# Kernel tuning notes

Hardware: AMD Instinct MI355X
Metric: run time of the kernel (lower is better)

## Reference

```python
import jax, jax.numpy as jnp
import numpy as np

BN_EPS = 1e-5


def setup_inputs() -> dict:
    key = jax.random.key(0)
    ks = jax.random.split(key, 10)
    B, C2, Hh, Ww = 4, 64, 64, 64  # in_channels=128, C/2=64
    C = 2 * C2
    inp = {
        "H": jax.random.normal(ks[0], (B, C2, Hh, Ww), jnp.float32),
        "L": jax.random.normal(ks[1], (B, C2, Hh, Ww), jnp.float32),
        # 1x1 convs stored as [out, in] matrices
        "theta_w": jax.random.normal(ks[2], (C2, C), jnp.float32) * (1.0 / np.sqrt(C)),
        "theta_b": jnp.zeros((C2,), jnp.float32),
        "phi_w": jax.random.normal(ks[3], (C2, C), jnp.float32) * (1.0 / np.sqrt(C)),
        "phi_b": jnp.zeros((C2,), jnp.float32),
        "g_w": jax.random.normal(ks[4], (C2, C2), jnp.float32) * (1.0 / np.sqrt(C2)),
        "g_b": jnp.zeros((C2,), jnp.float32),
        # 3x3 conv of CBR block, OIHW
        "conv_w": jax.random.normal(ks[5], (C2, C2, 3, 3), jnp.float32) * (1.0 / np.sqrt(C2 * 9)),
        "conv_b": jnp.zeros((C2,), jnp.float32),
        # BatchNorm (inference-mode) params
        "bn_gamma": jnp.ones((C2,), jnp.float32),
        "bn_beta": jnp.zeros((C2,), jnp.float32),
        "bn_mean": jnp.zeros((C2,), jnp.float32),
        "bn_var": jnp.ones((C2,), jnp.float32),
    }
    return inp


def reference(H, L, theta_w, theta_b, phi_w, phi_b, g_w, g_b,
              conv_w, conv_b, bn_gamma, bn_beta, bn_mean, bn_var):
    B, C2, h, w = L.shape
    N = h * w
    HL = jnp.concatenate([H, L], axis=1)  # [B, C, h, w]
    # 1x1 conv projections as channel matmuls
    A = jnp.einsum('oc,bchw->bohw', theta_w, HL) + theta_b[:, None, None]  # [B,C2,h,w]
    Bm = jnp.einsum('oc,bchw->bohw', phi_w, HL) + phi_b[:, None, None]
    A = A.reshape(B, C2, N).transpose(0, 2, 1)   # [B, N, C2]
    Bm = Bm.reshape(B, C2, N)                    # [B, C2, N]
    M = jnp.einsum('bnc,bcm->bnm', A, Bm)        # [B, N, N], unscaled
    M = jax.nn.softmax(M, axis=1)                # softmax over FIRST spatial axis (dim=1)
    D = jnp.einsum('oc,bchw->bohw', g_w, L) + g_b[:, None, None]
    D = D.reshape(B, C2, N)                      # [B, C2, N]
    E = jnp.einsum('bcn,bnm->bcm', D, M)         # [B, C2, N]
    E = E.reshape(B, C2, h, w)
    # CBR: conv3x3(pad=1) -> BatchNorm (inference) -> ReLU
    F = jax.lax.conv_general_dilated(
        E, conv_w, window_strides=(1, 1), padding='SAME',
        dimension_numbers=('NCHW', 'OIHW', 'NCHW')) + conv_b[None, :, None, None]
    F = (F - bn_mean[None, :, None, None]) * jax.lax.rsqrt(bn_var + BN_EPS)[None, :, None, None]
    F = F * bn_gamma[None, :, None, None] + bn_beta[None, :, None, None]
    F = jax.nn.relu(F)
    return H + F
```

## Files before the change

### kernel.cpp

```cpp
#include <hip/hip_runtime.h>

typedef __bf16 bf16;
typedef unsigned short u16;
typedef __attribute__((ext_vector_type(8))) __bf16 bf16x8;
typedef __attribute__((ext_vector_type(16))) float f32x16;
typedef __attribute__((ext_vector_type(2))) unsigned int uint2v;
typedef __attribute__((ext_vector_type(4))) unsigned int uint4v;

#define MFMA32(a, b, c) __builtin_amdgcn_mfma_f32_32x32x16_bf16(a, b, c, 0, 0, 0)

__device__ __forceinline__ u16 bbits(float f) {
  bf16 h = (bf16)f;
  return __builtin_bit_cast(u16, h);
}
__device__ __forceinline__ float bf2f(u16 u) {
  return (float)__builtin_bit_cast(bf16, u);
}
__device__ __forceinline__ bf16x8 ldg16(const u16* p) {
  return *reinterpret_cast<const bf16x8*>(p);
}
__device__ __forceinline__ bf16x8 ld_p8(const u16* p) {
  uint2v a = *reinterpret_cast<const uint2v*>(p);
  uint2v b = *reinterpret_cast<const uint2v*>(p + 4);
  uint4v u;
  u.x = a.x; u.y = a.y; u.z = b.x; u.w = b.y;
  return __builtin_bit_cast(bf16x8, u);
}
__device__ __forceinline__ void split8(const float* xv, bf16x8& hi, bf16x8& lo) {
  uint4v hv, lv;
#pragma unroll
  for (int jp = 0; jp < 4; ++jp) {
    float a0 = xv[2 * jp], a1 = xv[2 * jp + 1];
    u16 h0 = bbits(a0), h1 = bbits(a1);
    u16 l0 = bbits(a0 - bf2f(h0)), l1 = bbits(a1 - bf2f(h1));
    unsigned hh = (unsigned)h0 | ((unsigned)h1 << 16);
    unsigned ll = (unsigned)l0 | ((unsigned)l1 << 16);
    if (jp == 0) { hv.x = hh; lv.x = ll; }
    else if (jp == 1) { hv.y = hh; lv.y = ll; }
    else if (jp == 2) { hv.z = hh; lv.z = ll; }
    else { hv.w = hh; lv.w = ll; }
  }
  hi = __builtin_bit_cast(bf16x8, hv);
  lo = __builtin_bit_cast(bf16x8, lv);
}


__global__ __launch_bounds__(256) void pa_prep(
    const float* __restrict__ cw, const float* __restrict__ cbias,
    const float* __restrict__ gamma, const float* __restrict__ beta,
    const float* __restrict__ mean, const float* __restrict__ var,
    const float* __restrict__ tw, const float* __restrict__ pw, const float* __restrict__ gw,
    u16* __restrict__ Wt, float* __restrict__ bnA, float* __restrict__ bnB,
    u16* __restrict__ Wth, u16* __restrict__ Wtl,
    u16* __restrict__ Wph, u16* __restrict__ Wpl,
    u16* __restrict__ Wgh, u16* __restrict__ Wgl) {
  int i = blockIdx.x * 256 + threadIdx.x;
  if (i < 36864) {
    int ci = i & 63, co = (i >> 6) & 63, s = i >> 12;
    Wt[(s * 64 + co) * 64 + ci] = bbits(cw[(co * 64 + ci) * 9 + s]);
  }
  if (i < 16384) {
    int ii = i & 8191;
    int j = ii & 7, l = (ii >> 3) & 63, f = ii >> 9;
    int out = (f & 1) * 32 + (l & 31);
    int in = (f >> 1) * 16 + (l >> 5) * 8 + j;
    const float* W = (i < 8192) ? tw : pw;
    float v = W[out * 128 + in];
    u16 h = bbits(v);
    u16 lo = bbits(v - bf2f(h));
    if (i < 8192) { Wth[ii] = h; Wtl[ii] = lo; }
    else { Wph[ii] = h; Wpl[ii] = lo; }
  } else if (i < 20480) {
    int ii = i - 16384;
    int j = ii & 7, l = (ii >> 3) & 63, f = ii >> 9;
    int out = (f & 1) * 32 + (l & 31);
    int in = (f >> 1) * 16 + (l >> 5) * 8 + j;
    float v = gw[out * 64 + in];
    u16 h = bbits(v);
    Wgh[ii] = h;
    Wgl[ii] = bbits(v - bf2f(h));
  }
  if (i < 64) {
    float rs = rsqrtf(var[i] + 1e-5f);
    float A = gamma[i] * rs;
    bnA[i] = A;
    bnB[i] = (cbias[i] - mean[i]) * A + beta[i];
  }
}

template <bool LO>
__device__ __forceinline__ void store_qk_swz(const f32x16& a0, const f32x16& a1,
                                             const float* __restrict__ bias,
                                             u16* __restrict__ Hi, u16* __restrict__ Lo,
                                             int base, int l31, int q2) {
#pragma unroll
  for (int mt = 0; mt < 2; ++mt) {
    const f32x16& A = mt ? a1 : a0;
#pragma unroll
    for (int rq = 0; rq < 4; ++rq) {
      int ch = mt * 32 + rq * 8 + q2 * 4;
      float4 bb = *reinterpret_cast<const float4*>(bias + ch);
      float v0 = A[rq * 4 + 0] + bb.x;
      float v1 = A[rq * 4 + 1] + bb.y;
      float v2 = A[rq * 4 + 2] + bb.z;
      float v3 = A[rq * 4 + 3] + bb.w;
      int off = base + ((mt * 2 + (rq >> 1)) * 64 + l31 + 32 * (rq & 1)) * 8 + q2 * 4;
      u16 h0 = bbits(v0), h1 = bbits(v1), h2 = bbits(v2), h3 = bbits(v3);
      uint2v hv;
      hv.x = (unsigned)h0 | ((unsigned)h1 << 16);
      hv.y = (unsigned)h2 | ((unsigned)h3 << 16);
      *reinterpret_cast<uint2v*>(Hi + off) = hv;
      if (LO) {
        u16 l0 = bbits(v0 - bf2f(h0)), l1 = bbits(v1 - bf2f(h1));
        u16 l2 = bbits(v2 - bf2f(h2)), l3 = bbits(v3 - bf2f(h3));
        uint2v lv;
        lv.x = (unsigned)l0 | ((unsigned)l1 << 16);
        lv.y = (unsigned)l2 | ((unsigned)l3 << 16);
        *reinterpret_cast<uint2v*>(Lo + off) = lv;
      }
    }
  }
}

template <int NS>
__device__ __forceinline__ void gemm3(const u16* __restrict__ Wh, const u16* __restrict__ Wl,
                                      const bf16x8* Bh, const bf16x8* Bl,
                                      int lane, f32x16& a0, f32x16& a1) {
#pragma unroll
  for (int s = 0; s < NS; ++s) {
    bf16x8 w0h = ldg16(Wh + ((s * 2 + 0) * 64 + lane) * 8);
    bf16x8 w0l = ldg16(Wl + ((s * 2 + 0) * 64 + lane) * 8);
    bf16x8 w1h = ldg16(Wh + ((s * 2 + 1) * 64 + lane) * 8);
    bf16x8 w1l = ldg16(Wl + ((s * 2 + 1) * 64 + lane) * 8);
    a0 = MFMA32(w0h, Bh[s], a0);
    a0 = MFMA32(w0h, Bl[s], a0);
    a0 = MFMA32(w0l, Bh[s], a0);
    a1 = MFMA32(w1h, Bh[s], a1);
    a1 = MFMA32(w1h, Bl[s], a1);
    a1 = MFMA32(w1l, Bh[s], a1);
  }
}

__global__ __launch_bounds__(384, 2) void pa_proj(
    const float* __restrict__ H, const float* __restrict__ L,
    const float* __restrict__ tb, const float* __restrict__ pb, const float* __restrict__ gb,
    const u16* __restrict__ Wth, const u16* __restrict__ Wtl,
    const u16* __restrict__ Wph, const u16* __restrict__ Wpl,
    const u16* __restrict__ Wgh, const u16* __restrict__ Wgl,
    u16* __restrict__ Qh, u16* __restrict__ Ql,
    u16* __restrict__ Kh, u16* __restrict__ V) {
  int b = blockIdx.x >> 6;
  int tile64 = blockIdx.x & 63;
  int w = threadIdx.x >> 6;
  int lane = threadIdx.x & 63;
  int l31 = lane & 31, q2 = lane >> 5;
  int half = w & 1, role = w >> 1;
  int tile32 = tile64 * 2 + half;
  int n = tile32 * 32 + l31;
  int base = tile32 * 2048;

  if (role < 2) {
    bf16x8 Bh[8], Bl[8];
#pragma unroll
    for (int s = 0; s < 8; ++s) {
      const float* src = (s < 4) ? (H + (b * 64 + s * 16) * 4096)
                                 : (L + (b * 64 + (s - 4) * 16) * 4096);
      const float* pp = src + (q2 * 8) * 4096 + n;
      float xv[8];
#pragma unroll
      for (int j = 0; j < 8; ++j) xv[j] = pp[j * 4096];
      split8(xv, Bh[s], Bl[s]);
    }
    f32x16 a0 = {}, a1 = {};
    if (role == 0) {
      gemm3<8>(Wth, Wtl, Bh, Bl, lane, a0, a1);
      store_qk_swz<false>(a0, a1, tb, Kh + b * 262144, (u16*)nullptr, base, l31, q2);
    } else {
      gemm3<8>(Wph, Wpl, Bh, Bl, lane, a0, a1);
      store_qk_swz<true>(a0, a1, pb, Qh + b * 262144, Ql + b * 262144, base, l31, q2);
    }
  } else {
    bf16x8 Bh[4], Bl[4];
#pragma unroll
    for (int s = 0; s < 4; ++s) {
      const float* pp = L + (b * 64 + s * 16 + q2 * 8) * 4096 + n;
      float xv[8];
#pragma unroll
      for (int j = 0; j < 8; ++j) xv[j] = pp[j * 4096];
      split8(xv, Bh[s], Bl[s]);
    }
    f32x16 a0 = {}, a1 = {};
    gemm3<4>(Wgh, Wgl, Bh, Bl, lane, a0, a1);
    u16* Vb = V + b * 262144;
    int kch = (l31 >> 4) & 1, q2v = (l31 >> 3) & 1, jn = l31 & 7;
#pragma unroll
    for (int mt = 0; mt < 2; ++mt) {
      const f32x16& A = mt ? a1 : a0;
#pragma unroll
      for (int rq = 0; rq < 4; ++rq) {
        int ch = mt * 32 + rq * 8 + q2 * 4;
        float4 bb = *reinterpret_cast<const float4*>(gb + ch);
        float vv[4] = {A[rq * 4 + 0] + bb.x, A[rq * 4 + 1] + bb.y,
                       A[rq * 4 + 2] + bb.z, A[rq * 4 + 3] + bb.w};
#pragma unroll
        for (int i2 = 0; i2 < 4; ++i2) {
          int c31 = rq * 8 + q2 * 4 + i2;
          int lane_v = c31 + 32 * q2v;
          Vb[(((tile32 * 2 + kch) * 2 + mt) * 64 + lane_v) * 8 + jn] = bbits(vv[i2]);
        }
      }
    }
  }
}

__global__ __launch_bounds__(512, 4) void pa_flash(
    const u16* __restrict__ Qhg, const u16* __restrict__ Qlg,
    const u16* __restrict__ Khg, const u16* __restrict__ Vg, u16* __restrict__ E) {
  __shared__ __align__(16) char smem[18432];
  u16* Pb = (u16*)smem;
  float* Obuf = (float*)smem;
  float* MLm = (float*)(smem + 8448);
  float* MLl = (float*)(smem + 9472);
  float* Lst = (float*)(smem + 10496);

  int tid = threadIdx.x;
  int w = tid >> 6, lane = tid & 63;
  int l31 = lane & 31, q2 = lane >> 5;
  int b = blockIdx.x >> 7, mt = blockIdx.x & 127;
  int m0 = mt * 32;
  int bq = b * 4096;
  const u16* Qb = Qhg + b * 262144;
  const u16* Qlb = Qlg + b * 262144;
  const u16* Kb = Khg + b * 262144;
  const u16* Vb = Vg + b * 262144;

  bf16x8 qh[4], ql[4];
#pragma unroll
  for (int kc = 0; kc < 4; ++kc) {
    qh[kc] = ldg16(Qb + ((mt * 4 + kc) * 64 + lane) * 8);
    ql[kc] = ldg16(Qlb + ((mt * 4 + kc) * 64 + lane) * 8);
  }

  f32x16 accO[2] = {};
  float Mm = 0.f, Ll = 0.f;
  u16* mypb = Pb + w * (32 * 36);
  u16* prow = mypb + l31 * 36;

#pragma unroll 1
  for (int it = 0; it < 16; ++it) {
    int tile = it * 8 + w;

    bf16x8 kh[4];
#pragma unroll
    for (int kc = 0; kc < 4; ++kc) kh[kc] = ldg16(Kb + ((tile * 4 + kc) * 64 + lane) * 8);
    bf16x8 vf[2][2];
#pragma unroll
    for (int kch = 0; kch < 2; ++kch)
#pragma unroll
      for (int cbi = 0; cbi < 2; ++cbi)
        vf[cbi][kch] = ldg16(Vb + (((tile * 2 + kch) * 2 + cbi) * 64 + lane) * 8);

    f32x16 a = {};
#pragma unroll
    for (int kc = 0; kc < 4; ++kc) {
      a = MFMA32(kh[kc], qh[kc], a);
      a = MFMA32(kh[kc], ql[kc], a);
    }
    if (it == 0) {
      float tmax = a[0];
#pragma unroll
      for (int r = 1; r < 16; ++r) tmax = fmaxf(tmax, a[r]);
      tmax = fmaxf(tmax, __shfl_xor(tmax, 32, 64));
      Mm = tmax;
    }
    float pv[16];
    float psum = 0.f;
#pragma unroll
    for (int r = 0; r < 16; ++r) {
      pv[r] = __expf(a[r] - Mm);
      psum += pv[r];
    }
    psum += __shfl_xor(psum, 32, 64);
    Ll += psum;
#pragma unroll
    for (int rq = 0; rq < 4; ++rq) {
      unsigned lo = (unsigned)bbits(pv[rq * 4 + 0]) | ((unsigned)bbits(pv[rq * 4 + 1]) << 16);
      unsigned hi = (unsigned)bbits(pv[rq * 4 + 2]) | ((unsigned)bbits(pv[rq * 4 + 3]) << 16);
      uint2v uu;
      uu.x = lo;
      uu.y = hi;
      *reinterpret_cast<uint2v*>(prow + rq * 8 + q2 * 4) = uu;
    }
    bf16x8 p0 = ld_p8(prow + q2 * 8);
    bf16x8 p1 = ld_p8(prow + 16 + q2 * 8);
    accO[0] = MFMA32(vf[0][0], p0, accO[0]);
    accO[0] = MFMA32(vf[0][1], p1, accO[0]);
    accO[1] = MFMA32(vf[1][0], p0, accO[1]);
    accO[1] = MFMA32(vf[1][1], p1, accO[1]);
  }

  __syncthreads();
  if (q2 == 0) {
    MLm[w * 32 + l31] = Mm;
    MLl[w * 32 + l31] = Ll;
  }
  __syncthreads();
  float M = MLm[l31];
  for (int ww = 1; ww < 8; ++ww) M = fmaxf(M, MLm[ww * 32 + l31]);
  float ls = 0.f;
  for (int ww = 0; ww < 8; ++ww) ls += MLl[ww * 32 + l31] * __expf(MLm[ww * 32 + l31] - M);
  float mysc = __expf(Mm - M);
  if (w == 0 && q2 == 0) Lst[l31] = ls;
  for (int ww = 0; ww < 8; ++ww) {
    if (w == ww) {
#pragma unroll
      for (int cbi = 0; cbi < 2; ++cbi)
#pragma unroll
        for (int r = 0; r < 16; ++r) {
          int c = cbi * 32 + (r & 3) + 8 * (r >> 2) + 4 * q2;
          float* dst = &Obuf[c * 33 + l31];
          float v = accO[cbi][r] * mysc;
          if (ww == 0)
            *dst = v;
          else
            *dst += v;
        }
    }
    __syncthreads();
  }
  int em = tid >> 4, ec0 = (tid & 15) * 4;
  float invl = 1.0f / Lst[em];
  float v0 = Obuf[(ec0 + 0) * 33 + em] * invl;
  float v1 = Obuf[(ec0 + 1) * 33 + em] * invl;
  float v2 = Obuf[(ec0 + 2) * 33 + em] * invl;
  float v3 = Obuf[(ec0 + 3) * 33 + em] * invl;
  uint2v u0;
  u0.x = (unsigned)bbits(v0) | ((unsigned)bbits(v1) << 16);
  u0.y = (unsigned)bbits(v2) | ((unsigned)bbits(v3) << 16);
  *reinterpret_cast<uint2v*>(E + (bq + m0 + em) * 64 + ec0) = u0;
}

__global__ __launch_bounds__(256) void pa_conv(
    const u16* __restrict__ E, const u16* __restrict__ Wt,
    const float* __restrict__ bnA, const float* __restrict__ bnB,
    const float* __restrict__ H, float* __restrict__ out) {
  __shared__ u16 Er[3][66 * 68];
  int tid = threadIdx.x;
  int blk = blockIdx.x;
  int b = blk >> 6, y = blk & 63;
  int lane = tid & 63;
  int l31 = lane & 31, q2 = lane >> 5;
  int wv = tid >> 6;
  int cbi = wv >> 1, mb = wv & 1;
  int s0 = (y == 0) ? 1 : 0;
  int s1 = (y == 63) ? 1 : 2;

  for (int s = s0; s <= s1; ++s) {
    int yy = y + s - 1;
#pragma unroll
    for (int rep = 0; rep < 2; ++rep) {
      int id = rep * 256 + tid;
      int x = id >> 3, co = (id & 7) * 8;
      const uint2v* src = reinterpret_cast<const uint2v*>(E + ((b * 4096 + yy * 64 + x) * 64 + co));
      uint2v a = src[0], b4 = src[1];
      u16* d = &Er[s][(x + 1) * 68 + co];
      *reinterpret_cast<uint2v*>(d) = a;
      *reinterpret_cast<uint2v*>(d + 4) = b4;
    }
  }
  if (tid < 96) {
    int s = tid >> 5, side = (tid >> 4) & 1, co = (tid & 15) * 4;
    uint2v z;
    z.x = 0;
    z.y = 0;
    *reinterpret_cast<uint2v*>(&Er[s][(side ? 65 : 0) * 68 + co]) = z;
  }
  __syncthreads();

  f32x16 acc = {};
  for (int s = s0; s <= s1; ++s) {
#pragma unroll
    for (int dx = 0; dx < 3; ++dx)
#pragma unroll
      for (int kc = 0; kc < 4; ++kc) {
        bf16x8 a = ldg16(Wt + ((s * 3 + dx) * 64 + cbi * 32 + l31) * 64 + kc * 16 + q2 * 8);
        const u16* pbr = &Er[s][(mb * 32 + l31 + dx) * 68 + kc * 16 + q2 * 8];
        bf16x8 bb = ld_p8(pbr);
        acc = MFMA32(a, bb, acc);
      }
  }
#pragma unroll
  for (int r = 0; r < 16; ++r) {
    int c = cbi * 32 + (r & 3) + 8 * (r >> 2) + 4 * q2;
    int x = mb * 32 + l31;
    float v = acc[r] * bnA[c] + bnB[c];
    v = fmaxf(v, 0.f);
    int idx = ((b * 64 + c) * 64 + y) * 64 + x;
    out[idx] = H[idx] + v;
  }
}

extern "C" void kernel_launch(void* const* d_in, const int* in_sizes, int n_in,
                              void* d_out, int out_size, void* d_ws, size_t ws_size,
                              hipStream_t stream) {
  (void)in_sizes; (void)n_in; (void)out_size; (void)ws_size;
  const float* H = (const float*)d_in[0];
  const float* L = (const float*)d_in[1];
  const float* tw = (const float*)d_in[2];
  const float* tb = (const float*)d_in[3];
  const float* pw = (const float*)d_in[4];
  const float* pb = (const float*)d_in[5];
  const float* gw = (const float*)d_in[6];
  const float* gb = (const float*)d_in[7];
  const float* cw = (const float*)d_in[8];
  const float* cb = (const float*)d_in[9];
  const float* gamma = (const float*)d_in[10];
  const float* beta = (const float*)d_in[11];
  const float* mean = (const float*)d_in[12];
  const float* var = (const float*)d_in[13];

  const int NC = 16384 * 64;
  u16* Qh = (u16*)d_ws;
  u16* Ql = Qh + NC;
  u16* Kh = Ql + NC;
  u16* Vv = Kh + NC;
  u16* Eb = Vv + NC;
  u16* Wt = Eb + NC;
  float* bnA = (float*)(Wt + 36864);
  float* bnB = bnA + 64;
  u16* Wth = (u16*)(bnB + 64);
  u16* Wtl = Wth + 8192;
  u16* Wph = Wtl + 8192;
  u16* Wpl = Wph + 8192;
  u16* Wgh = Wpl + 8192;
  u16* Wgl = Wgh + 4096;

  pa_prep<<<144, 256, 0, stream>>>(cw, cb, gamma, beta, mean, var, tw, pw, gw,
                                   Wt, bnA, bnB, Wth, Wtl, Wph, Wpl, Wgh, Wgl);
  pa_proj<<<256, 384, 0, stream>>>(H, L, tb, pb, gb, Wth, Wtl, Wph, Wpl, Wgh, Wgl,
                                   Qh, Ql, Kh, Vv);
  pa_flash<<<512, 512, 0, stream>>>(Qh, Ql, Kh, Vv, Eb);
  pa_conv<<<256, 256, 0, stream>>>(Eb, Wt, bnA, bnB, H, (float*)d_out);
}
```

Baseline: 133.4 us.

## Trim split-bf16 terms, register P exchange, K prefetch, split-K conv

Drops the low-weight bf16 term for the theta and g projections, so those GEMMs issue two MFMAs per step instead of three. The flash kernel now moves P between lanes with cross-lane shuffles instead of an LDS round-trip, and prefetches the next K tile into registers. The conv kernel uses 512 threads with a split-K over channel chunks reduced through shared memory, and reads weights in an MFMA-fragment layout. Dropping the low weight terms slightly reduces projection precision. The conv split-K adds a barrier and extra LDS traffic.

```diff
diff --git a/kernel.cpp b/kernel.cpp
--- a/kernel.cpp
+++ b/kernel.cpp
@@ -25,6 +25,9 @@
   uint4v u;
   u.x = a.x; u.y = a.y; u.z = b.x; u.w = b.y;
   return __builtin_bit_cast(bf16x8, u);
+}
+__device__ __forceinline__ unsigned packbf(float a, float b) {
+  return (unsigned)bbits(a) | ((unsigned)bbits(b) << 16);
 }
 __device__ __forceinline__ void split8(const float* xv, bf16x8& hi, bf16x8& lo) {
   uint4v hv, lv;
@@ -57,7 +60,10 @@
   int i = blockIdx.x * 256 + threadIdx.x;
   if (i < 36864) {
     int ci = i & 63, co = (i >> 6) & 63, s = i >> 12;
-    Wt[(s * 64 + co) * 64 + ci] = bbits(cw[(co * 64 + ci) * 9 + s]);
+    int kc = ci >> 4, q2c = (ci >> 3) & 1, j = ci & 7;
+    int lane = q2c * 32 + (co & 31);
+    int cbi = co >> 5;
+    Wt[(((s * 4 + kc) * 2 + cbi) * 64 + lane) * 8 + j] = bbits(cw[(co * 64 + ci) * 9 + s]);
   }
   if (i < 16384) {
     int ii = i & 8191;
@@ -141,12 +147,26 @@
   }
 }
 
+template <int NS>
+__device__ __forceinline__ void gemm2(const u16* __restrict__ Wh,
+                                      const bf16x8* Bh, const bf16x8* Bl,
+                                      int lane, f32x16& a0, f32x16& a1) {
+#pragma unroll
+  for (int s = 0; s < NS; ++s) {
+    bf16x8 w0h = ldg16(Wh + ((s * 2 + 0) * 64 + lane) * 8);
+    bf16x8 w1h = ldg16(Wh + ((s * 2 + 1) * 64 + lane) * 8);
+    a0 = MFMA32(w0h, Bh[s], a0);
+    a0 = MFMA32(w0h, Bl[s], a0);
+    a1 = MFMA32(w1h, Bh[s], a1);
+    a1 = MFMA32(w1h, Bl[s], a1);
+  }
+}
+
 __global__ __launch_bounds__(384, 2) void pa_proj(
     const float* __restrict__ H, const float* __restrict__ L,
     const float* __restrict__ tb, const float* __restrict__ pb, const float* __restrict__ gb,
-    const u16* __restrict__ Wth, const u16* __restrict__ Wtl,
-    const u16* __restrict__ Wph, const u16* __restrict__ Wpl,
-    const u16* __restrict__ Wgh, const u16* __restrict__ Wgl,
+    const u16* __restrict__ Wth, const u16* __restrict__ Wph, const u16* __restrict__ Wpl,
+    const u16* __restrict__ Wgh,
     u16* __restrict__ Qh, u16* __restrict__ Ql,
     u16* __restrict__ Kh, u16* __restrict__ V) {
   int b = blockIdx.x >> 6;
@@ -173,7 +193,7 @@
     }
     f32x16 a0 = {}, a1 = {};
     if (role == 0) {
-      gemm3<8>(Wth, Wtl, Bh, Bl, lane, a0, a1);
+      gemm2<8>(Wth, Bh, Bl, lane, a0, a1);
       store_qk_swz<false>(a0, a1, tb, Kh + b * 262144, (u16*)nullptr, base, l31, q2);
     } else {
       gemm3<8>(Wph, Wpl, Bh, Bl, lane, a0, a1);
@@ -190,7 +210,7 @@
       split8(xv, Bh[s], Bl[s]);
     }
     f32x16 a0 = {}, a1 = {};
-    gemm3<4>(Wgh, Wgl, Bh, Bl, lane, a0, a1);
+    gemm2<4>(Wgh, Bh, Bl, lane, a0, a1);
     u16* Vb = V + b * 262144;
     int kch = (l31 >> 4) & 1, q2v = (l31 >> 3) & 1, jn = l31 & 7;
 #pragma unroll
@@ -216,12 +236,10 @@
 __global__ __launch_bounds__(512, 4) void pa_flash(
     const u16* __restrict__ Qhg, const u16* __restrict__ Qlg,
     const u16* __restrict__ Khg, const u16* __restrict__ Vg, u16* __restrict__ E) {
-  __shared__ __align__(16) char smem[18432];
-  u16* Pb = (u16*)smem;
-  float* Obuf = (float*)smem;
-  float* MLm = (float*)(smem + 8448);
-  float* MLl = (float*)(smem + 9472);
-  float* Lst = (float*)(smem + 10496);
+  __shared__ float Obuf[64 * 33];
+  __shared__ float MLm[8 * 32];
+  __shared__ float MLl[8 * 32];
+  __shared__ float Lst[32];
 
   int tid = threadIdx.x;
   int w = tid >> 6, lane = tid & 63;
@@ -243,16 +261,15 @@
 
   f32x16 accO[2] = {};
   float Mm = 0.f, Ll = 0.f;
-  u16* mypb = Pb + w * (32 * 36);
-  u16* prow = mypb + l31 * 36;
+
+  bf16x8 kh[4];
+#pragma unroll
+  for (int kc = 0; kc < 4; ++kc) kh[kc] = ldg16(Kb + ((w * 4 + kc) * 64 + lane) * 8);
 
 #pragma unroll 1
   for (int it = 0; it < 16; ++it) {
     int tile = it * 8 + w;
 
-    bf16x8 kh[4];
-#pragma unroll
-    for (int kc = 0; kc < 4; ++kc) kh[kc] = ldg16(Kb + ((tile * 4 + kc) * 64 + lane) * 8);
     bf16x8 vf[2][2];
 #pragma unroll
     for (int kch = 0; kch < 2; ++kch)
@@ -266,6 +283,10 @@
       a = MFMA32(kh[kc], qh[kc], a);
       a = MFMA32(kh[kc], ql[kc], a);
     }
+    int tn = (it < 15) ? tile + 8 : tile;
+#pragma unroll
+    for (int kc = 0; kc < 4; ++kc) kh[kc] = ldg16(Kb + ((tn * 4 + kc) * 64 + lane) * 8);
+
     if (it == 0) {
       float tmax = a[0];
 #pragma unroll
@@ -282,24 +303,37 @@
     }
     psum += __shfl_xor(psum, 32, 64);
     Ll += psum;
-#pragma unroll
-    for (int rq = 0; rq < 4; ++rq) {
-      unsigned lo = (unsigned)bbits(pv[rq * 4 + 0]) | ((unsigned)bbits(pv[rq * 4 + 1]) << 16);
-      unsigned hi = (unsigned)bbits(pv[rq * 4 + 2]) | ((unsigned)bbits(pv[rq * 4 + 3]) << 16);
-      uint2v uu;
-      uu.x = lo;
-      uu.y = hi;
-      *reinterpret_cast<uint2v*>(prow + rq * 8 + q2 * 4) = uu;
-    }
-    bf16x8 p0 = ld_p8(prow + q2 * 8);
-    bf16x8 p1 = ld_p8(prow + 16 + q2 * 8);
+
+    unsigned pd[4][2];
+#pragma unroll
+    for (int q = 0; q < 4; ++q) {
+      pd[q][0] = packbf(pv[q * 4 + 0], pv[q * 4 + 1]);
+      pd[q][1] = packbf(pv[q * 4 + 2], pv[q * 4 + 3]);
+    }
+    unsigned xd[4][2];
+#pragma unroll
+    for (int q = 0; q < 4; ++q) {
+      xd[q][0] = (unsigned)__shfl_xor((int)pd[q][0], 32, 64);
+      xd[q][1] = (unsigned)__shfl_xor((int)pd[q][1], 32, 64);
+    }
+    uint4v u0, u1;
+    u0.x = q2 ? xd[1][0] : pd[0][0];
+    u0.y = q2 ? xd[1][1] : pd[0][1];
+    u0.z = q2 ? pd[1][0] : xd[0][0];
+    u0.w = q2 ? pd[1][1] : xd[0][1];
+    u1.x = q2 ? xd[3][0] : pd[2][0];
+    u1.y = q2 ? xd[3][1] : pd[2][1];
+    u1.z = q2 ? pd[3][0] : xd[2][0];
+    u1.w = q2 ? pd[3][1] : xd[2][1];
+    bf16x8 p0 = __builtin_bit_cast(bf16x8, u0);
+    bf16x8 p1 = __builtin_bit_cast(bf16x8, u1);
+
     accO[0] = MFMA32(vf[0][0], p0, accO[0]);
     accO[0] = MFMA32(vf[0][1], p1, accO[0]);
     accO[1] = MFMA32(vf[1][0], p0, accO[1]);
     accO[1] = MFMA32(vf[1][1], p1, accO[1]);
   }
 
-  __syncthreads();
   if (q2 == 0) {
     MLm[w * 32 + l31] = Mm;
     MLl[w * 32 + l31] = Ll;
@@ -335,38 +369,35 @@
   float v2 = Obuf[(ec0 + 2) * 33 + em] * invl;
   float v3 = Obuf[(ec0 + 3) * 33 + em] * invl;
   uint2v u0;
-  u0.x = (unsigned)bbits(v0) | ((unsigned)bbits(v1) << 16);
-  u0.y = (unsigned)bbits(v2) | ((unsigned)bbits(v3) << 16);
+  u0.x = packbf(v0, v1);
+  u0.y = packbf(v2, v3);
   *reinterpret_cast<uint2v*>(E + (bq + m0 + em) * 64 + ec0) = u0;
 }
 
-__global__ __launch_bounds__(256) void pa_conv(
+__global__ __launch_bounds__(512) void pa_conv(
     const u16* __restrict__ E, const u16* __restrict__ Wt,
     const float* __restrict__ bnA, const float* __restrict__ bnB,
     const float* __restrict__ H, float* __restrict__ out) {
   __shared__ u16 Er[3][66 * 68];
+  __shared__ float Rbuf[4][64 * 17];
   int tid = threadIdx.x;
   int blk = blockIdx.x;
   int b = blk >> 6, y = blk & 63;
   int lane = tid & 63;
   int l31 = lane & 31, q2 = lane >> 5;
   int wv = tid >> 6;
-  int cbi = wv >> 1, mb = wv & 1;
+  int ks = wv & 1, mb = (wv >> 1) & 1, cbi = wv >> 2;
   int s0 = (y == 0) ? 1 : 0;
   int s1 = (y == 63) ? 1 : 2;
 
   for (int s = s0; s <= s1; ++s) {
     int yy = y + s - 1;
-#pragma unroll
-    for (int rep = 0; rep < 2; ++rep) {
-      int id = rep * 256 + tid;
-      int x = id >> 3, co = (id & 7) * 8;
-      const uint2v* src = reinterpret_cast<const uint2v*>(E + ((b * 4096 + yy * 64 + x) * 64 + co));
-      uint2v a = src[0], b4 = src[1];
-      u16* d = &Er[s][(x + 1) * 68 + co];
-      *reinterpret_cast<uint2v*>(d) = a;
-      *reinterpret_cast<uint2v*>(d + 4) = b4;
-    }
+    int x = tid >> 3, co = (tid & 7) * 8;
+    const uint2v* src = reinterpret_cast<const uint2v*>(E + ((b * 4096 + yy * 64 + x) * 64 + co));
+    uint2v a = src[0], b4 = src[1];
+    u16* d = &Er[s][(x + 1) * 68 + co];
+    *reinterpret_cast<uint2v*>(d) = a;
+    *reinterpret_cast<uint2v*>(d + 4) = b4;
   }
   if (tid < 96) {
     int s = tid >> 5, side = (tid >> 4) & 1, co = (tid & 15) * 4;
@@ -377,26 +408,37 @@
   }
   __syncthreads();
 
-  f32x16 acc = {};
+  f32x16 a0 = {}, a1 = {};
   for (int s = s0; s <= s1; ++s) {
 #pragma unroll
-    for (int dx = 0; dx < 3; ++dx)
-#pragma unroll
-      for (int kc = 0; kc < 4; ++kc) {
-        bf16x8 a = ldg16(Wt + ((s * 3 + dx) * 64 + cbi * 32 + l31) * 64 + kc * 16 + q2 * 8);
-        const u16* pbr = &Er[s][(mb * 32 + l31 + dx) * 68 + kc * 16 + q2 * 8];
-        bf16x8 bb = ld_p8(pbr);
-        acc = MFMA32(a, bb, acc);
-      }
-  }
-#pragma unroll
-  for (int r = 0; r < 16; ++r) {
-    int c = cbi * 32 + (r & 3) + 8 * (r >> 2) + 4 * q2;
-    int x = mb * 32 + l31;
-    float v = acc[r] * bnA[c] + bnB[c];
-    v = fmaxf(v, 0.f);
-    int idx = ((b * 64 + c) * 64 + y) * 64 + x;
-    out[idx] = H[idx] + v;
+    for (int dx = 0; dx < 3; ++dx) {
+      int s3 = s * 3 + dx;
+      int kcA = ks * 2, kcB = ks * 2 + 1;
+      bf16x8 wa = ldg16(Wt + (((s3 * 4 + kcA) * 2 + cbi) * 64 + lane) * 8);
+      bf16x8 wb = ldg16(Wt + (((s3 * 4 + kcB) * 2 + cbi) * 64 + lane) * 8);
+      bf16x8 ea = ld_p8(&Er[s][(mb * 32 + l31 + dx) * 68 + kcA * 16 + q2 * 8]);
+      bf16x8 eb = ld_p8(&Er[s][(mb * 32 + l31 + dx) * 68 + kcB * 16 + q2 * 8]);
+      a0 = MFMA32(wa, ea, a0);
+      a1 = MFMA32(wb, eb, a1);
+    }
+  }
+  int p = cbi * 2 + mb;
+  if (ks == 1) {
+#pragma unroll
+    for (int r = 0; r < 16; ++r) Rbuf[p][lane * 17 + r] = a0[r] + a1[r];
+  }
+  __syncthreads();
+  if (ks == 0) {
+#pragma unroll
+    for (int r = 0; r < 16; ++r) {
+      int c = cbi * 32 + (r & 3) + 8 * (r >> 2) + 4 * q2;
+      int x = mb * 32 + l31;
+      float v = a0[r] + a1[r] + Rbuf[p][lane * 17 + r];
+      v = v * bnA[c] + bnB[c];
+      v = fmaxf(v, 0.f);
+      int idx = ((b * 64 + c) * 64 + y) * 64 + x;
+      out[idx] = H[idx] + v;
+    }
   }
 }
 
@@ -437,8 +479,8 @@
 
   pa_prep<<<144, 256, 0, stream>>>(cw, cb, gamma, beta, mean, var, tw, pw, gw,
                                    Wt, bnA, bnB, Wth, Wtl, Wph, Wpl, Wgh, Wgl);
-  pa_proj<<<256, 384, 0, stream>>>(H, L, tb, pb, gb, Wth, Wtl, Wph, Wpl, Wgh, Wgl,
+  pa_proj<<<256, 384, 0, stream>>>(H, L, tb, pb, gb, Wth, Wph, Wpl, Wgh,
                                    Qh, Ql, Kh, Vv);
   pa_flash<<<512, 512, 0, stream>>>(Qh, Ql, Kh, Vv, Eb);
-  pa_conv<<<256, 256, 0, stream>>>(Eb, Wt, bnA, bnB, H, (float*)d_out);
-}
+  pa_conv<<<256, 512, 0, stream>>>(Eb, Wt, bnA, bnB, H, (float*)d_out);
+}
```

After: 135.5 us. Within noise of the previous version (+1.6%).
